# Kernel tuning notes

Measured on AMD Instinct MI355X. Metric: run time of the kernel, lower is better.

Reference implementation:

```python
import jax, jax.numpy as jnp
import numpy as np


def setup_inputs() -> dict:
    key = jax.random.key(0)
    ks = jax.random.split(key, 7)
    B, C, T = 64, 2048, 256  # T must equal C // heads (see module's matmul(attn, v))
    s = 0.02
    return {
        "x": jax.random.normal(ks[0], (B, C, T), dtype=jnp.float32),
        "Wq": jax.random.normal(ks[1], (C, C), dtype=jnp.float32) * s,
        "bq": jax.random.normal(ks[2], (C,), dtype=jnp.float32) * s,
        "Wk": jax.random.normal(ks[3], (C, C), dtype=jnp.float32) * s,
        "bk": jax.random.normal(ks[4], (C,), dtype=jnp.float32) * s,
        "Wv": jax.random.normal(ks[5], (C, C), dtype=jnp.float32) * s,
        "bv": jax.random.normal(ks[6], (C,), dtype=jnp.float32) * s,
        "heads": 8,
    }


def reference(x, Wq, bq, Wk, bk, Wv, bv, heads):
    B, C, T = x.shape
    H = heads
    D = C // H  # must equal T for this module's math
    scale = float(D) ** -0.5

    def proj(W, b):
        # 1x1 Conv1d == per-timestep linear: out[b,o,t] = sum_c W[o,c] x[b,c,t] + b[o]
        return jnp.einsum('oc,bct->bot', W, x) + b[None, :, None]

    q = proj(Wq, bq).reshape(B, H, D, T).transpose(0, 1, 3, 2)  # (B,H,T,D)
    k = proj(Wk, bk).reshape(B, H, D, T).transpose(0, 1, 3, 2)  # (B,H,T,D)
    v = proj(Wv, bv).reshape(B, H, D, T)                         # (B,H,D,T), D==T

    attn = jax.nn.softmax(jnp.einsum('bhid,bhjd->bhij', q, k) * scale, axis=-1)  # (B,H,T,T)
    # Faithful to torch: matmul(attn, v) with v UNpermuted -> contract attn's last axis with v's D axis
    out = jnp.einsum('bhik,bhkj->bhij', attn, v)  # (B,H,T,T)
    return out.reshape(B, C, T)
```

## Files before the change

kernel.cpp:

```cpp
#include <hip/hip_runtime.h>


typedef __attribute__((ext_vector_type(8))) short    bf16x8;
typedef __attribute__((ext_vector_type(4))) float    f32x4;
typedef __attribute__((ext_vector_type(4))) unsigned short us4;
typedef __attribute__((ext_vector_type(8))) unsigned short us8;
typedef unsigned short u16;
typedef unsigned int   u32;

#define CC 2048
#define TT 256
#define BB 64
#define HH 8
#define DD 256

__device__ __forceinline__ u16 f2bf(float f) {
  u32 u = __builtin_bit_cast(u32, f);
  u32 r = (u + 0x7fffu + ((u >> 16) & 1u)) >> 16;
  return (u16)r;
}
__device__ __forceinline__ float bf2f(u16 b) {
  u32 u = ((u32)b) << 16;
  return __builtin_bit_cast(float, u);
}

__device__ __forceinline__ void async16(const void* g, void* l) {
  __builtin_amdgcn_global_load_lds(
      (const __attribute__((address_space(1))) u32*)g,
      (__attribute__((address_space(3))) u32*)l, 16, 0, 0);
}

__global__ __launch_bounds__(256) void wconv_kernel(
    const float* __restrict__ w0, const float* __restrict__ w1,
    const float* __restrict__ w2, u16* __restrict__ dst) {
  int p = blockIdx.y;
  const float* s = (p == 0) ? w0 : (p == 1) ? w1 : w2;
  size_t i = ((size_t)blockIdx.x * 256 + threadIdx.x) * 4;
  float4 v = *(const float4*)(s + i);
  us4 o = {f2bf(v.x), f2bf(v.y), f2bf(v.z), f2bf(v.w)};
  *(us4*)(dst + (size_t)p * CC * CC + i) = o;
}

__global__ __launch_bounds__(256) void xt_kernel(
    const float* __restrict__ x, u16* __restrict__ xT) {
  __shared__ float tile[64][68];
  int t0 = blockIdx.x * 64;
  int c0 = blockIdx.y * 64;
  int b  = blockIdx.z;
  int tid = threadIdx.x;
  int lr = tid >> 4;
  int lc = (tid & 15) * 4;
  const float* src = x + ((size_t)b * CC + c0) * TT + t0;
#pragma unroll
  for (int s = 0; s < 4; ++s) {
    int c = s * 16 + lr;
    float4 v = *(const float4*)(src + (size_t)c * TT + lc);
    *(float4*)&tile[c][lc] = v;
  }
  __syncthreads();
  int t  = tid >> 2;
  int cb = (tid & 3) * 16;
  u16 tmp[16];
#pragma unroll
  for (int e = 0; e < 16; ++e) tmp[e] = f2bf(tile[cb + e][t]);
  u16* dst = xT + ((size_t)b * TT + t0 + t) * CC + c0 + cb;
  *(us8*)dst       = *(const us8*)&tmp[0];
  *(us8*)(dst + 8) = *(const us8*)&tmp[8];
}

__global__ __launch_bounds__(512, 2) void proj_kernel(
    const u16* __restrict__ Wbf, const u16* __restrict__ xT,
    const float* __restrict__ bq, const float* __restrict__ bk,
    const float* __restrict__ bv, u16* __restrict__ qkv) {
  __shared__ __align__(16) u16 As[2][16384];
  __shared__ __align__(16) u16 Bs[2][16384];

  int tid = threadIdx.x;
  int bid = blockIdx.x;
  int wg  = (bid & 7) * 192 + (bid >> 3);
  int pm  = wg >> 6;
  int b   = wg & 63;
  int proj = pm >> 3;
  int mt   = pm & 7;
  int m0   = mt << 8;

  const u16* Ap = Wbf + (size_t)proj * CC * CC + (size_t)m0 * CC;
  const u16* Xp = xT + (size_t)b * TT * CC;
  const float* bias = (proj == 0) ? bq : (proj == 1) ? bk : bv;

  int lane = tid & 63, w = tid >> 6;
  int wm = w >> 2, wn = w & 3;
  int ar = lane & 15, kq = lane >> 4;

  int r_b = tid >> 3;
  int c8  = tid & 7;
  int c8s = c8 ^ (r_b & 7);
  const size_t go = (size_t)r_b * CC + (size_t)c8s * 8;
  const int ldsq = r_b * 64 + c8 * 8;

  const int cx = (kq ^ (ar & 7)) * 8;

  const int arow = wm * 16 + ar;
  const int brow = wn * 16 + ar;

#define STG_A(buf, kt, h)                                                     \
  do {                                                                        \
    async16(Ap + (size_t)((h) * 128) * CC + (size_t)(kt) * 64 + go,           \
            &As[buf][(h) * 8192 + ldsq]);                                     \
    async16(Ap + (size_t)((h) * 128 + 64) * CC + (size_t)(kt) * 64 + go,      \
            &As[buf][(h) * 8192 + 4096 + ldsq]);                              \
  } while (0)
#define STG_B(buf, kt, h)                                                     \
  do {                                                                        \
    async16(Xp + (size_t)((h) * 128) * CC + (size_t)(kt) * 64 + go,           \
            &Bs[buf][(h) * 8192 + ldsq]);                                     \
    async16(Xp + (size_t)((h) * 128 + 64) * CC + (size_t)(kt) * 64 + go,      \
            &Bs[buf][(h) * 8192 + 4096 + ldsq]);                              \
  } while (0)

  bf16x8 af[4][2], bfr[4][2];
  f32x4 acc[8][4] = {};

#define LDA(buf, mh)                                                          \
  do {                                                                        \
    _Pragma("unroll") for (int fl = 0; fl < 4; ++fl) {                        \
      int row = ((mh) * 4 + fl) * 32 + arow;                                  \
      af[fl][0] = *(const bf16x8*)&As[buf][row * 64 + cx];                    \
      af[fl][1] = *(const bf16x8*)&As[buf][row * 64 + (cx ^ 32)];             \
    }                                                                         \
  } while (0)
#define LDBALL(buf)                                                           \
  do {                                                                        \
    _Pragma("unroll") for (int g = 0; g < 4; ++g) {                           \
      int row = g * 64 + brow;                                                \
      bfr[g][0] = *(const bf16x8*)&Bs[buf][row * 64 + cx];                    \
      bfr[g][1] = *(const bf16x8*)&Bs[buf][row * 64 + (cx ^ 32)];             \
    }                                                                         \
  } while (0)
#define MMA_MH(mh)                                                            \
  do {                                                                        \
    _Pragma("unroll") for (int fl = 0; fl < 4; ++fl) {                        \
      _Pragma("unroll") for (int g = 0; g < 4; ++g) {                         \
        acc[(mh) * 4 + fl][g] = __builtin_amdgcn_mfma_f32_16x16x32_bf16(      \
            af[fl][0], bfr[g][0], acc[(mh) * 4 + fl][g], 0, 0, 0);            \
        acc[(mh) * 4 + fl][g] = __builtin_amdgcn_mfma_f32_16x16x32_bf16(      \
            af[fl][1], bfr[g][1], acc[(mh) * 4 + fl][g], 0, 0, 0);            \
      }                                                                       \
    }                                                                         \
  } while (0)
#define POSTF(mh)                                                             \
  do {                                                                        \
    __builtin_amdgcn_s_barrier();                                             \
    asm volatile("s_waitcnt lgkmcnt(0)" ::: "memory");                        \
    __builtin_amdgcn_sched_barrier(0);                                        \
    __builtin_amdgcn_s_setprio(1);                                            \
    MMA_MH(mh);                                                               \
    __builtin_amdgcn_s_setprio(0);                                            \
    __builtin_amdgcn_sched_barrier(0);                                        \
    __builtin_amdgcn_s_barrier();                                             \
  } while (0)
#define VM4 asm volatile("s_waitcnt vmcnt(4)" ::: "memory")
#define VM0 asm volatile("s_waitcnt vmcnt(0)" ::: "memory")

  STG_A(0, 0, 0); STG_B(0, 0, 0); STG_A(0, 0, 1); STG_B(0, 0, 1);
  STG_A(1, 1, 0); STG_B(1, 1, 0);
  VM4;
  __builtin_amdgcn_s_barrier();

  for (int i = 0; i < 15; ++i) {
    int k = 2 * i;
    LDA(0, 0); LDBALL(0);
    STG_B(1, k + 1, 1); STG_A(1, k + 1, 1);
    POSTF(0);
    LDA(0, 1);
    STG_A(0, k + 2, 0); STG_B(0, k + 2, 0);
    VM4;
    POSTF(1);
    LDA(1, 0); LDBALL(1);
    STG_B(0, k + 2, 1); STG_A(0, k + 2, 1);
    POSTF(0);
    LDA(1, 1);
    STG_A(1, k + 3, 0); STG_B(1, k + 3, 0);
    VM4;
    POSTF(1);
  }
  LDA(0, 0); LDBALL(0);
  STG_B(1, 31, 1); STG_A(1, 31, 1);
  POSTF(0);
  LDA(0, 1);
  VM0;
  POSTF(1);
  LDA(1, 0); LDBALL(1);
  POSTF(0);
  LDA(1, 1);
  POSTF(1);

  u16* outp = qkv + (size_t)proj * BB * CC * TT +
              (size_t)(b * HH + mt) * TT * DD;
#pragma unroll
  for (int f = 0; f < 8; ++f) {
    int d0 = f * 32 + wm * 16 + kq * 4;
    float b0 = bias[m0 + d0],     b1 = bias[m0 + d0 + 1];
    float b2 = bias[m0 + d0 + 2], b3 = bias[m0 + d0 + 3];
#pragma unroll
    for (int g = 0; g < 4; ++g) {
      int t = g * 64 + wn * 16 + ar;
      f32x4 v = acc[f][g];
      us4 pk = {f2bf(v[0] + b0), f2bf(v[1] + b1), f2bf(v[2] + b2),
                f2bf(v[3] + b3)};
      *(us4*)(outp + (size_t)t * DD + d0) = pk;
    }
  }
#undef STG_A
#undef STG_B
#undef LDA
#undef LDBALL
#undef MMA_MH
#undef POSTF
#undef VM4
#undef VM0
}

__global__ __launch_bounds__(256) void attn_kernel(
    const u16* __restrict__ qkv, float* __restrict__ out) {
  __shared__ __align__(16) u16 As[64 * 32];
  __shared__ __align__(16) u16 Bs[256 * 32];
  __shared__ __align__(16) u16 Ps[64 * 264];
  __shared__ float rowpart[64][4];
  __shared__ float inv[64];

  int tid = threadIdx.x;
  int i0 = blockIdx.x * 64;
  int bh = blockIdx.y;
  const size_t hd = (size_t)TT * DD;
  const u16* Q = qkv + (size_t)bh * hd;
  const u16* K = qkv + (size_t)(BB * HH + bh) * hd;
  const u16* V = qkv + (size_t)(2 * BB * HH + bh) * hd;

  int lane = tid & 63, w = tid >> 6;
  int ar = lane & 15, kq = lane >> 4;
  int arow = tid >> 2, acol = (tid & 3) * 8;

  const u16* Qbase = Q + (size_t)(i0 + arow) * DD + acol;
  const u16* Kbase = K + (size_t)arow * DD + acol;
  const u16* Vbase = V + (size_t)arow * DD + acol;

  f32x4 acc[4][4] = {};
  for (int k0 = 0; k0 < DD; k0 += 32) {
    async16(Qbase + k0, As + tid * 8);
#pragma unroll
    for (int s = 0; s < 4; ++s)
      async16(Kbase + (size_t)(s * 64) * DD + k0, Bs + s * 2048 + tid * 8);
    __syncthreads();
    bf16x8 af[4], bfv[4];
#pragma unroll
    for (int mt = 0; mt < 4; ++mt)
      af[mt] = *(const bf16x8*)&As[(mt * 16 + ar) * 32 + kq * 8];
#pragma unroll
    for (int nt = 0; nt < 4; ++nt)
      bfv[nt] = *(const bf16x8*)&Bs[(w * 64 + nt * 16 + ar) * 32 + kq * 8];
#pragma unroll
    for (int mt = 0; mt < 4; ++mt)
#pragma unroll
      for (int nt = 0; nt < 4; ++nt)
        acc[mt][nt] = __builtin_amdgcn_mfma_f32_16x16x32_bf16(
            af[mt], bfv[nt], acc[mt][nt], 0, 0, 0);
    __syncthreads();
  }
  const float scale = 0.0625f;
#pragma unroll
  for (int mt = 0; mt < 4; ++mt) {
    float ps[4] = {0.f, 0.f, 0.f, 0.f};
#pragma unroll
    for (int nt = 0; nt < 4; ++nt) {
      f32x4 v = acc[mt][nt];
#pragma unroll
      for (int r = 0; r < 4; ++r) {
        float p = __expf(v[r] * scale);
        u16 pb = f2bf(p);
        Ps[(mt * 16 + kq * 4 + r) * 264 + (w * 64 + nt * 16 + ar)] = pb;
        ps[r] += bf2f(pb);
      }
    }
#pragma unroll
    for (int r = 0; r < 4; ++r) {
      float s = ps[r];
      s += __shfl_xor(s, 1, 64);
      s += __shfl_xor(s, 2, 64);
      s += __shfl_xor(s, 4, 64);
      s += __shfl_xor(s, 8, 64);
      if (ar == 0) rowpart[mt * 16 + kq * 4 + r][w] = s;
    }
  }
  __syncthreads();
  if (tid < 64) {
    float s = rowpart[tid][0] + rowpart[tid][1] + rowpart[tid][2] +
              rowpart[tid][3];
    inv[tid] = 1.0f / s;
  }
#pragma unroll
  for (int mt = 0; mt < 4; ++mt)
#pragma unroll
    for (int nt = 0; nt < 4; ++nt) acc[mt][nt] = (f32x4){0.f, 0.f, 0.f, 0.f};
  for (int k0 = 0; k0 < TT; k0 += 32) {
#pragma unroll
    for (int s = 0; s < 4; ++s)
      async16(Vbase + (size_t)(s * 64) * DD + k0, Bs + s * 2048 + tid * 8);
    __syncthreads();
    bf16x8 af[4], bfv[4];
#pragma unroll
    for (int mt = 0; mt < 4; ++mt)
      af[mt] = *(const bf16x8*)&Ps[(mt * 16 + ar) * 264 + k0 + kq * 8];
#pragma unroll
    for (int nt = 0; nt < 4; ++nt)
      bfv[nt] = *(const bf16x8*)&Bs[(w * 64 + nt * 16 + ar) * 32 + kq * 8];
#pragma unroll
    for (int mt = 0; mt < 4; ++mt)
#pragma unroll
      for (int nt = 0; nt < 4; ++nt)
        acc[mt][nt] = __builtin_amdgcn_mfma_f32_16x16x32_bf16(
            af[mt], bfv[nt], acc[mt][nt], 0, 0, 0);
    __syncthreads();
  }
  int b = bh >> 3, h = bh & 7;
  float* obase = out + ((size_t)b * CC + h * TT + i0) * TT;
#pragma unroll
  for (int mt = 0; mt < 4; ++mt)
#pragma unroll
    for (int r = 0; r < 4; ++r) {
      int m = mt * 16 + kq * 4 + r;
      float iv = inv[m];
#pragma unroll
      for (int nt = 0; nt < 4; ++nt) {
        int n = w * 64 + nt * 16 + ar;
        obase[(size_t)m * TT + n] = acc[mt][nt][r] * iv;
      }
    }
}

extern "C" void kernel_launch(void* const* d_in, const int* in_sizes, int n_in,
                              void* d_out, int out_size, void* d_ws,
                              size_t ws_size, hipStream_t stream) {
  const float* x  = (const float*)d_in[0];
  const float* Wq = (const float*)d_in[1];
  const float* bq = (const float*)d_in[2];
  const float* Wk = (const float*)d_in[3];
  const float* bk = (const float*)d_in[4];
  const float* Wv = (const float*)d_in[5];
  const float* bv = (const float*)d_in[6];
  float* out = (float*)d_out;

  char* ws = (char*)d_ws;
  u16* xT  = (u16*)ws;
  u16* Wbf = (u16*)(ws + 67108864);
  u16* qkv = (u16*)(ws + 67108864 + 25165824);

  wconv_kernel<<<dim3(4096, 3, 1), 256, 0, stream>>>(Wq, Wk, Wv, Wbf);
  xt_kernel<<<dim3(4, 32, 64), 256, 0, stream>>>(x, xT);
  proj_kernel<<<dim3(1536, 1, 1), 512, 0, stream>>>(Wbf, xT, bq, bk, bv, qkv);
  attn_kernel<<<dim3(4, 512, 1), 256, 0, stream>>>(qkv, out);
}
```

Measured before the change: 814.7 us.

## Restructure projection GEMM pipeline to drop trailing barrier and reorder global prefetches

```diff
diff --git a/kernel.cpp b/kernel.cpp
--- a/kernel.cpp
+++ b/kernel.cpp
@@ -148,52 +148,53 @@
       }                                                                       \
     }                                                                         \
   } while (0)
-#define POSTF(mh)                                                             \
+#define BARLG                                                                 \
   do {                                                                        \
     __builtin_amdgcn_s_barrier();                                             \
     asm volatile("s_waitcnt lgkmcnt(0)" ::: "memory");                        \
     __builtin_amdgcn_sched_barrier(0);                                        \
+  } while (0)
+#define MM(mh)                                                                \
+  do {                                                                        \
     __builtin_amdgcn_s_setprio(1);                                            \
     MMA_MH(mh);                                                               \
     __builtin_amdgcn_s_setprio(0);                                            \
     __builtin_amdgcn_sched_barrier(0);                                        \
-    __builtin_amdgcn_s_barrier();                                             \
-  } while (0)
-#define VM4 asm volatile("s_waitcnt vmcnt(4)" ::: "memory")
+  } while (0)
+#define VM6 asm volatile("s_waitcnt vmcnt(6)" ::: "memory")
+#define VM2 asm volatile("s_waitcnt vmcnt(2)" ::: "memory")
 #define VM0 asm volatile("s_waitcnt vmcnt(0)" ::: "memory")
 
-  STG_A(0, 0, 0); STG_B(0, 0, 0); STG_A(0, 0, 1); STG_B(0, 0, 1);
-  STG_A(1, 1, 0); STG_B(1, 1, 0);
-  VM4;
+  STG_A(0, 0, 0); STG_B(0, 0, 0); STG_B(0, 0, 1);
+  STG_A(0, 0, 1);
+  VM2;
   __builtin_amdgcn_s_barrier();
 
   for (int i = 0; i < 15; ++i) {
     int k = 2 * i;
+    STG_A(1, k + 1, 0); STG_B(1, k + 1, 0); STG_B(1, k + 1, 1);
     LDA(0, 0); LDBALL(0);
-    STG_B(1, k + 1, 1); STG_A(1, k + 1, 1);
-    POSTF(0);
+    VM6; BARLG; MM(0);
+    STG_A(1, k + 1, 1);
     LDA(0, 1);
-    STG_A(0, k + 2, 0); STG_B(0, k + 2, 0);
-    VM4;
-    POSTF(1);
+    VM2; BARLG; MM(1);
+    STG_A(0, k + 2, 0); STG_B(0, k + 2, 0); STG_B(0, k + 2, 1);
     LDA(1, 0); LDBALL(1);
-    STG_B(0, k + 2, 1); STG_A(0, k + 2, 1);
-    POSTF(0);
+    VM6; BARLG; MM(0);
+    STG_A(0, k + 2, 1);
     LDA(1, 1);
-    STG_A(1, k + 3, 0); STG_B(1, k + 3, 0);
-    VM4;
-    POSTF(1);
-  }
+    VM2; BARLG; MM(1);
+  }
+  STG_A(1, 31, 0); STG_B(1, 31, 0); STG_B(1, 31, 1);
   LDA(0, 0); LDBALL(0);
-  STG_B(1, 31, 1); STG_A(1, 31, 1);
-  POSTF(0);
+  VM6; BARLG; MM(0);
+  STG_A(1, 31, 1);
   LDA(0, 1);
-  VM0;
-  POSTF(1);
+  VM2; BARLG; MM(1);
   LDA(1, 0); LDBALL(1);
-  POSTF(0);
+  VM0; BARLG; MM(0);
   LDA(1, 1);
-  POSTF(1);
+  BARLG; MM(1);
 
   u16* outp = qkv + (size_t)proj * BB * CC * TT +
               (size_t)(b * HH + mt) * TT * DD;
@@ -216,8 +217,10 @@
 #undef LDA
 #undef LDBALL
 #undef MMA_MH
-#undef POSTF
-#undef VM4
+#undef BARLG
+#undef MM
+#undef VM6
+#undef VM2
 #undef VM0
 }
 
```

Result: no change. 829.8 us (+1.9%).
